# Kernel tuning notes

Hardware: AMD Instinct MI355X
Metric: run time of the kernel (lower is better)

Reference implementation:

```python
import jax, jax.numpy as jnp
import numpy as np
from jax import lax

C, CMID, RED, SCALE, KUP, KENC = 128, 64, 8, 2, 5, 3


def _conv(x, w, b=None, pad=0, groups=1):
    y = lax.conv_general_dilated(x, w, (1, 1), [(pad, pad), (pad, pad)],
                                 feature_group_count=groups,
                                 dimension_numbers=('NCHW', 'OIHW', 'NCHW'))
    if b is not None:
        y = y + b[None, :, None, None]
    return y


def setup_inputs() -> dict:
    key = jax.random.key(0)
    ks = jax.random.split(key, 8)
    s = 0.05
    return {
        'X': jax.random.normal(ks[0], (2, C, 64, 64), jnp.float32),
        'w3': jax.random.normal(ks[1], (CMID, C, 3, 3), jnp.float32) * s,
        'b3': jnp.zeros((CMID,), jnp.float32),
        'w5': jax.random.normal(ks[2], (CMID, C, 5, 5), jnp.float32) * s,
        'b5': jnp.zeros((CMID,), jnp.float32),
        'wa1': jax.random.normal(ks[3], (CMID // RED, CMID, 1, 1), jnp.float32) * s,
        'ba1': jnp.zeros((CMID // RED,), jnp.float32),
        'wa2': jax.random.normal(ks[4], (CMID, CMID // RED, 1, 1), jnp.float32) * s,
        'ba2': jnp.zeros((CMID,), jnp.float32),
        'wedge': jax.random.normal(ks[5], (CMID, 1, 3, 3), jnp.float32) * s,
        'wenc': jax.random.normal(ks[6], ((SCALE * KUP) ** 2, CMID, KENC, KENC), jnp.float32) * s,
    }


def reference(X, w3, b3, w5, b5, wa1, ba1, wa2, ba2, wedge, wenc):
    b, c, h, w = X.shape
    h_, w_ = h * SCALE, w * SCALE

    # kernel-prediction branch: 3x3 + 5x5 compression convs
    W = _conv(X, w3, b3, pad=1) + _conv(X, w5, b5, pad=2)

    # DetailEnhanceAttention: SE-style channel gate + depthwise edge conv
    avg = jnp.mean(W, axis=(2, 3), keepdims=True)            # (b, cmid, 1, 1)
    a = _conv(avg, wa1, ba1, pad=0)
    a = jax.nn.sigmoid(_conv(a, wa2, ba2, pad=0))
    edge = _conv(W, wedge, None, pad=1, groups=CMID)          # depthwise 3x3
    W = W * a + edge

    # encoder conv -> (b, (scale*k_up)^2, h, w)
    W = _conv(W, wenc, None, pad=KENC // 2)

    # PixelShuffle(scale): channels (k_up^2, r, r) -> (k_up^2, h*r, w*r)
    Wp = W.reshape(b, KUP * KUP, SCALE, SCALE, h, w)
    Wp = Wp.transpose(0, 1, 4, 2, 5, 3).reshape(b, KUP * KUP, h_, w_)
    Wp = jax.nn.softmax(Wp, axis=1)                           # softmax over k_up^2 taps

    # nearest upsample of X to (b, c, h_, w_)
    Xu = jnp.repeat(jnp.repeat(X, SCALE, axis=2), SCALE, axis=3)

    # unfold: kernel=k_up, dilation=scale, padding=k_up//2*scale
    p = (KUP // 2) * SCALE
    Xpad = jnp.pad(Xu, ((0, 0), (0, 0), (p, p), (p, p)))
    # (b, c, k_up^2, h_, w_), tap index = ki*k_up + kj (torch unfold order)
    patches = jnp.stack([
        Xpad[:, :, i * SCALE:i * SCALE + h_, j * SCALE:j * SCALE + w_]
        for i in range(KUP) for j in range(KUP)
    ], axis=2)

    out = jnp.einsum('bkhw,bckhw->bchw', Wp, patches)
    return out
```

## Files before the change

### kernel.cpp

```cpp
#include <hip/hip_runtime.h>
#include <math.h>

typedef __attribute__((ext_vector_type(2))) _Float16 f16x2;
typedef __attribute__((ext_vector_type(4))) _Float16 f16x4;
typedef __attribute__((ext_vector_type(8))) _Float16 f16x8;
typedef __attribute__((ext_vector_type(4))) float f32x4;

#if __has_builtin(__builtin_amdgcn_fdot2)
#define FDOT2(a, b, c) __builtin_amdgcn_fdot2((a), (b), (c), false)
#else
static __device__ __forceinline__ float FDOT2(f16x2 a, f16x2 b, float c) {
  return c + (float)a[0] * (float)b[0] + (float)a[1] * (float)b[1];
}
#endif

#define XPAD8_B  0
#define WFC_B    2506752
#define WFE_B    2916352
#define WFEATP_B 3045376
#define WEDGET_B 4194304
#define BCOMB_B  4195456
#define AVG_B    4195712

__global__ __launch_bounds__(256) void prep_kernel(
    const float* __restrict__ X,
    const float* __restrict__ w3, const float* __restrict__ b3,
    const float* __restrict__ w5, const float* __restrict__ b5,
    const float* __restrict__ wedge, const float* __restrict__ wenc,
    char* __restrict__ wsb) {
  int idx = blockIdx.x * 256 + threadIdx.x;
  if (idx < 156672) {
    int x = idx % 72;
    int t = idx / 72;
    int y = t % 68;
    int t2 = t / 68;
    int gg = t2 & 15, b = t2 >> 4;
    int yy = y - 2, xx = x - 2;
    bool ok = (yy >= 0 && yy < 64 && xx >= 0 && xx < 64);
    f16x8 h;
#pragma unroll
    for (int j = 0; j < 8; ++j) {
      float v = ok ? X[((b * 128 + gg * 8 + j) << 12) + yy * 64 + xx] : 0.f;
      h[j] = (_Float16)v;
    }
    ((f16x8*)(wsb + XPAD8_B))[idx] = h;
  }
  if (idx < 25600) {
    int l = idx & 63;
    int q = idx >> 6;
    int ntg = q & 3;
    int q2 = q >> 2;
    int cc = q2 & 3;
    int t = q2 >> 2;
    int ky = t / 5, kx = t % 5;
    int oc = ntg * 16 + (l & 15);
    int ci0 = cc * 32 + (l >> 4) * 8;
    f16x8 h;
#pragma unroll
    for (int i = 0; i < 8; ++i) {
      int ci = ci0 + i;
      float v = w5[(oc * 128 + ci) * 25 + t];
      if (ky >= 1 && ky <= 3 && kx >= 1 && kx <= 3)
        v += w3[(oc * 128 + ci) * 9 + (ky - 1) * 3 + (kx - 1)];
      h[i] = (_Float16)v;
    }
    ((f16x8*)(wsb + WFC_B))[idx] = h;
  }
  if (idx < 8064) {
    int l = idx & 63;
    int q = idx >> 6;
    int nt = q % 7;
    int q2 = q / 7;
    int cc = q2 & 1;
    int t = q2 >> 1;
    int oc = nt * 16 + (l & 15);
    int ci0 = cc * 32 + (l >> 4) * 8;
    f16x8 h;
#pragma unroll
    for (int i = 0; i < 8; ++i) {
      float v = (oc < 100) ? wenc[(oc * 64 + ci0 + i) * 9 + t] : 0.f;
      h[i] = (_Float16)v;
    }
    ((f16x8*)(wsb + WFE_B))[idx] = h;
  }
  if (idx < 6272) {
    int plane = idx / 392, p = idx % 392;
    int r, c;
    if (p < 136) {
      r = (p >= 68) ? 65 : 0;
      c = p % 68;
    } else {
      int q = p - 136;
      r = 1 + (q >> 2);
      int cm = q & 3;
      c = (cm == 0) ? 0 : (64 + cm);
    }
    f16x8 z = {(_Float16)0.f, (_Float16)0.f, (_Float16)0.f, (_Float16)0.f,
               (_Float16)0.f, (_Float16)0.f, (_Float16)0.f, (_Float16)0.f};
    *(f16x8*)((_Float16*)(wsb + WFEATP_B) + ((size_t)(plane * 66 + r) * 68 + c) * 8) = z;
  }
  if (idx < 72) {
    int k = idx >> 3, gg = idx & 7;
    f16x8 h;
#pragma unroll
    for (int j = 0; j < 8; ++j) h[j] = (_Float16)wedge[(gg * 8 + j) * 9 + k];
    ((f16x8*)(wsb + WEDGET_B))[idx] = h;
  }
  if (idx < 64) ((float*)(wsb + BCOMB_B))[idx] = b3[idx] + b5[idx];
  if (idx < 128) ((float*)(wsb + AVG_B))[idx] = b3[idx & 63] + b5[idx & 63];
}

__global__ __launch_bounds__(256) void convw_kernel(
    const _Float16* __restrict__ xpad8, const f16x8* __restrict__ wfc,
    const float* __restrict__ bcomb, _Float16* __restrict__ wfeatp,
    float* __restrict__ avg) {
  __shared__ __attribute__((aligned(16))) _Float16 xs[18560];
  __shared__ float red[64];
  const int tid = threadIdx.x;
  const int z = blockIdx.z;
  const int b = z >> 2, ntg = z & 3;
  const int tx0 = blockIdx.x * 8, ty0 = blockIdx.y * 8;

  for (int u = tid; u < 2304; u += 256) {
    int gg = u / 144;
    int rem = u - gg * 144;
    int r = rem / 12, c = rem - r * 12;
    f16x8 v = *(const f16x8*)&xpad8[((size_t)((b * 16 + gg) * 68 + ty0 + r) * 72 + tx0 + c) * 8];
    *(f16x8*)&xs[gg * 1160 + r * 96 + c * 8] = v;
  }
  __syncthreads();

  const int w = __builtin_amdgcn_readfirstlane(tid >> 6);
  const int l = tid & 63;
  const int lm = l & 15, lg = l >> 4;
  const int p = w * 16 + lm;
  const int abase = (p >> 3) * 96 + (p & 7) * 8;

  f32x4 accA = {0.f, 0.f, 0.f, 0.f}, accB = {0.f, 0.f, 0.f, 0.f};
  for (int dy = 0; dy < 5; ++dy) {
    for (int dx = 0; dx < 5; ++dx) {
      const int t = dy * 5 + dx;
      const int toff = abase + dy * 96 + dx * 8;
      const f16x8* wt = wfc + (t * 16 + ntg) * 64 + l;
#pragma unroll
      for (int cc = 0; cc < 4; ++cc) {
        f16x8 a = *(const f16x8*)&xs[(cc * 4 + lg) * 1160 + toff];
        f16x8 bb = wt[cc * 256];
        if (cc & 1)
          accB = __builtin_amdgcn_mfma_f32_16x16x32_f16(a, bb, accB, 0, 0, 0);
        else
          accA = __builtin_amdgcn_mfma_f32_16x16x32_f16(a, bb, accA, 0, 0, 0);
      }
    }
  }
  f32x4 acc = accA + accB;

  float s = acc[0] + acc[1] + acc[2] + acc[3];
  s += __shfl_xor(s, 16);
  s += __shfl_xor(s, 32);
  const float bias = bcomb[ntg * 16 + lm];
  __syncthreads();
#pragma unroll
  for (int r = 0; r < 4; ++r) {
    int pd = w * 16 + lg * 4 + r;
    xs[pd * 24 + lm] = (_Float16)(acc[r] + bias);
  }
  if (l < 16) red[w * 16 + lm] = s;
  __syncthreads();
  if (tid < 128) {
    int g2 = tid >> 6, pd = tid & 63;
    f16x8 v = *(const f16x8*)&xs[pd * 24 + g2 * 8];
    int gy = ty0 + (pd >> 3), gx = tx0 + (pd & 7);
    *(f16x8*)&wfeatp[((size_t)((b * 8 + ntg * 2 + g2) * 66 + 1 + gy) * 68 + 1 + gx) * 8] = v;
  }
  if (tid < 16) {
    float tot = red[tid] + red[16 + tid] + red[32 + tid] + red[48 + tid];
    atomicAdd(&avg[b * 64 + ntg * 16 + tid], tot * (1.f / 4096.f));
  }
}

#define SM_XT  0
#define SM_XSV 26880
#define SM_TS  34688
#define SM_SML 34688
#define SM_SMW 49536
#define SM_TOT 57216

__global__ __launch_bounds__(512) void enccarafe_kernel(
    const _Float16* __restrict__ wfeatp, const f16x8* __restrict__ wfe,
    const _Float16* __restrict__ xpad8, const f16x8* __restrict__ wedgeT,
    const float* __restrict__ wa1, const float* __restrict__ ba1,
    const float* __restrict__ wa2, const float* __restrict__ ba2,
    const float* __restrict__ avg, float* __restrict__ out) {
  __shared__ __attribute__((aligned(16))) char smem[SM_TOT];
  __shared__ f16x8 wedt[72];
  __shared__ float tlat[8];
  __shared__ float gsh[64];
  _Float16* xt = (_Float16*)(smem + SM_XT);
  _Float16* xsv = (_Float16*)(smem + SM_XSV);
  _Float16* ts = (_Float16*)(smem + SM_TS);
  float* sml = (float*)(smem + SM_SML);
  f16x2* smw2 = (f16x2*)(smem + SM_SMW);

  const int tid = threadIdx.x;
  const int b = blockIdx.z;
  const int tx0 = blockIdx.x * 8, ty0 = blockIdx.y * 4;

  for (int u = tid; u < 1664; u += 512) {
    int gg = u / 104;
    int rem = u - gg * 104;
    int r = rem / 13, c = rem - r * 13;
    f16x8 v = *(const f16x8*)&xpad8[((size_t)((b * 16 + gg) * 68 + ty0 + r) * 72 + tx0 + c) * 8];
    *(f16x8*)&xt[gg * 840 + r * 104 + c * 8] = v;
  }
  for (int u = tid; u < 768; u += 512) {
    int gg = u / 96;
    int rem = u - gg * 96;
    int r = rem / 12, c = rem - r * 12;
    int pr = ty0 - 1 + r, pc = tx0 - 1 + c;
    f16x8 v = {(_Float16)0.f, (_Float16)0.f, (_Float16)0.f, (_Float16)0.f,
               (_Float16)0.f, (_Float16)0.f, (_Float16)0.f, (_Float16)0.f};
    if (pr >= 0 && pr < 66 && pc >= 0 && pc < 68)
      v = *(const f16x8*)&wfeatp[((size_t)((b * 8 + gg) * 66 + pr) * 68 + pc) * 8];
    *(f16x8*)&ts[gg * 776 + r * 96 + c * 8] = v;
  }
  if (tid < 72) wedt[tid] = wedgeT[tid];
  if (tid < 8) {
    float s = ba1[tid];
    for (int i = 0; i < 64; ++i) s += wa1[tid * 64 + i] * avg[b * 64 + i];
    tlat[tid] = s;
  }
  __syncthreads();
  if (tid < 64) {
    float s = ba2[tid];
#pragma unroll
    for (int j = 0; j < 8; ++j) s += wa2[tid * 8 + j] * tlat[j];
    gsh[tid] = 1.f / (1.f + expf(-s));
  }
  __syncthreads();

  for (int u = tid; u < 480; u += 512) {
    int gg = u / 60;
    int rem = u - gg * 60;
    int r6 = rem / 10, c10 = rem - r6 * 10;
    int vy = ty0 - 1 + r6, vx = tx0 - 1 + c10;
    f16x8 res = {(_Float16)0.f, (_Float16)0.f, (_Float16)0.f, (_Float16)0.f,
                 (_Float16)0.f, (_Float16)0.f, (_Float16)0.f, (_Float16)0.f};
    if (vy >= 0 && vy < 64 && vx >= 0 && vx < 64) {
      float vout[8];
      f16x8 ctr = *(const f16x8*)&ts[gg * 776 + (r6 + 1) * 96 + (c10 + 1) * 8];
#pragma unroll
      for (int j = 0; j < 8; ++j) vout[j] = (float)ctr[j] * gsh[gg * 8 + j];
#pragma unroll
      for (int ky = 0; ky < 3; ++ky) {
#pragma unroll
        for (int kx = 0; kx < 3; ++kx) {
          int k = ky * 3 + kx;
          f16x8 tv = *(const f16x8*)&ts[gg * 776 + (r6 + ky) * 96 + (c10 + kx) * 8];
          f16x8 wv = wedt[k * 8 + gg];
#pragma unroll
          for (int j = 0; j < 8; ++j) vout[j] = fmaf((float)wv[j], (float)tv[j], vout[j]);
        }
      }
#pragma unroll
      for (int j = 0; j < 8; ++j) res[j] = (_Float16)vout[j];
    }
    *(f16x8*)&xsv[gg * 488 + r6 * 80 + c10 * 8] = res;
  }
  __syncthreads();

  {
    const int w = __builtin_amdgcn_readfirstlane(tid >> 6);
    const int l = tid & 63;
    const int pg = w & 1, hs = w >> 1;
    const int lm = l & 15, lg = l >> 4;
    const int p = pg * 16 + lm;
    const int abase = (p >> 3) * 80 + (p & 7) * 8;
    const int nt0 = hs * 2;
    const int ncnt = (hs == 3) ? 1 : 2;

    f32x4 a0 = {0.f, 0.f, 0.f, 0.f}, a1 = {0.f, 0.f, 0.f, 0.f};
    for (int dy = 0; dy < 3; ++dy) {
      for (int dx = 0; dx < 3; ++dx) {
        const int t = dy * 3 + dx;
        const int toff = abase + dy * 80 + dx * 8;
#pragma unroll
        for (int cc = 0; cc < 2; ++cc) {
          f16x8 a = *(const f16x8*)&xsv[(cc * 4 + lg) * 488 + toff];
          f16x8 b0 = wfe[((t * 2 + cc) * 7 + nt0) * 64 + l];
          a0 = __builtin_amdgcn_mfma_f32_16x16x32_f16(a, b0, a0, 0, 0, 0);
          if (ncnt == 2) {
            f16x8 b1 = wfe[((t * 2 + cc) * 7 + nt0 + 1) * 64 + l];
            a1 = __builtin_amdgcn_mfma_f32_16x16x32_f16(a, b1, a1, 0, 0, 0);
          }
        }
      }
    }
#pragma unroll
    for (int r = 0; r < 4; ++r) {
      int pd = pg * 16 + 4 * lg + r;
      sml[pd * 116 + nt0 * 16 + lm] = a0[r];
      if (ncnt == 2) sml[pd * 116 + (nt0 + 1) * 16 + lm] = a1[r];
    }
  }
  __syncthreads();

  if (tid < 128) {
    int pix = tid >> 2, sub = tid & 3;
    float lv[25];
    float m = -1e30f;
#pragma unroll
    for (int k = 0; k < 25; ++k) {
      lv[k] = sml[pix * 116 + k * 4 + sub];
      m = fmaxf(m, lv[k]);
    }
    float s = 0.f;
#pragma unroll
    for (int k = 0; k < 25; ++k) {
      lv[k] = __expf(lv[k] - m);
      s += lv[k];
    }
    float inv = 1.f / s;
#pragma unroll
    for (int ki = 0; ki < 5; ++ki) {
#pragma unroll
      for (int pr = 0; pr < 3; ++pr) {
        float wlo = lv[ki * 5 + 2 * pr] * inv;
        float whi = (2 * pr + 1 < 5) ? lv[ki * 5 + 2 * pr + 1] * inv : 0.f;
        f16x2 pk = {(_Float16)wlo, (_Float16)whi};
        smw2[((ki * 3 + pr) * 32 + pix) * 4 + sub] = pk;
      }
    }
  }
  __syncthreads();

  {
    const int slot = tid >> 5, pix = tid & 31;
    const int py = pix >> 3, px = pix & 7;
    const _Float16* xb = xt + slot * 840;

    float acc[4][8];
#pragma unroll
    for (int s = 0; s < 4; ++s)
#pragma unroll
      for (int j = 0; j < 8; ++j) acc[s][j] = 0.f;

    union U8 { f16x8 v; unsigned int u[4]; };
#pragma unroll
    for (int ki = 0; ki < 5; ++ki) {
      const _Float16* row = xb + (py + ki) * 104 + px * 8;
      U8 C[6];
#pragma unroll
      for (int c = 0; c < 6; ++c) C[c].v = *(const f16x8*)(row + c * 8);
#pragma unroll
      for (int pr = 0; pr < 3; ++pr) {
        const f16x2* wp = &smw2[((ki * 3 + pr) * 32 + pix) * 4];
        f16x2 w0 = wp[0], w1 = wp[1], w2 = wp[2], w3 = wp[3];
        const U8& A = C[2 * pr];
        const U8& B = C[2 * pr + 1];
#pragma unroll
        for (int k = 0; k < 4; ++k) {
          unsigned int lo = __builtin_amdgcn_perm(B.u[k], A.u[k], 0x05040100u);
          unsigned int hi = __builtin_amdgcn_perm(B.u[k], A.u[k], 0x07060302u);
          f16x2 xlo = __builtin_bit_cast(f16x2, lo);
          f16x2 xhi = __builtin_bit_cast(f16x2, hi);
          acc[0][2 * k] = FDOT2(w0, xlo, acc[0][2 * k]);
          acc[1][2 * k] = FDOT2(w1, xlo, acc[1][2 * k]);
          acc[2][2 * k] = FDOT2(w2, xlo, acc[2][2 * k]);
          acc[3][2 * k] = FDOT2(w3, xlo, acc[3][2 * k]);
          acc[0][2 * k + 1] = FDOT2(w0, xhi, acc[0][2 * k + 1]);
          acc[1][2 * k + 1] = FDOT2(w1, xhi, acc[1][2 * k + 1]);
          acc[2][2 * k + 1] = FDOT2(w2, xhi, acc[2][2 * k + 1]);
          acc[3][2 * k + 1] = FDOT2(w3, xhi, acc[3][2 * k + 1]);
        }
      }
    }
    int y0o = 2 * (ty0 + py), x0o = 2 * (tx0 + px);
#pragma unroll
    for (int j = 0; j < 8; ++j) {
      int c = slot * 8 + j;
      float* op = out + ((size_t)(b * 128 + c) * 128 + y0o) * 128 + x0o;
      float2 v0 = {acc[0][j], acc[1][j]};
      float2 v1 = {acc[2][j], acc[3][j]};
      *(float2*)op = v0;
      *(float2*)(op + 128) = v1;
    }
  }
}

extern "C" void kernel_launch(void* const* d_in, const int* in_sizes, int n_in,
                              void* d_out, int out_size, void* d_ws, size_t ws_size,
                              hipStream_t stream) {
  const float* X     = (const float*)d_in[0];
  const float* w3    = (const float*)d_in[1];
  const float* b3    = (const float*)d_in[2];
  const float* w5    = (const float*)d_in[3];
  const float* b5    = (const float*)d_in[4];
  const float* wa1   = (const float*)d_in[5];
  const float* ba1   = (const float*)d_in[6];
  const float* wa2   = (const float*)d_in[7];
  const float* ba2   = (const float*)d_in[8];
  const float* wedge = (const float*)d_in[9];
  const float* wenc  = (const float*)d_in[10];
  char* wsb = (char*)d_ws;
  float* out = (float*)d_out;

  _Float16* xpad8  = (_Float16*)(wsb + XPAD8_B);
  f16x8*    wfc    = (f16x8*)(wsb + WFC_B);
  f16x8*    wfe    = (f16x8*)(wsb + WFE_B);
  _Float16* wfeatp = (_Float16*)(wsb + WFEATP_B);
  f16x8*    wedgeT = (f16x8*)(wsb + WEDGET_B);
  float*    bcomb  = (float*)(wsb + BCOMB_B);
  float*    avg    = (float*)(wsb + AVG_B);

  prep_kernel<<<612, 256, 0, stream>>>(X, w3, b3, w5, b5, wedge, wenc, wsb);
  convw_kernel<<<dim3(8, 8, 8), 256, 0, stream>>>(xpad8, wfc, bcomb, wfeatp, avg);
  enccarafe_kernel<<<dim3(8, 16, 2), 512, 0, stream>>>(
      wfeatp, wfe, xpad8, wedgeT, wa1, ba1, wa2, ba2, avg, out);
}
```

Before: 47.65 us.

## Halve tile heights and split conv K across waves for more blocks

```diff
diff --git a/kernel.cpp b/kernel.cpp
--- a/kernel.cpp
+++ b/kernel.cpp
@@ -114,77 +114,86 @@
     const _Float16* __restrict__ xpad8, const f16x8* __restrict__ wfc,
     const float* __restrict__ bcomb, _Float16* __restrict__ wfeatp,
     float* __restrict__ avg) {
-  __shared__ __attribute__((aligned(16))) _Float16 xs[18560];
-  __shared__ float red[64];
+  __shared__ __attribute__((aligned(16))) _Float16 xs[16 * 776];
+  __shared__ float red[2][64][4];
+  __shared__ float redm[2][16];
   const int tid = threadIdx.x;
   const int z = blockIdx.z;
   const int b = z >> 2, ntg = z & 3;
-  const int tx0 = blockIdx.x * 8, ty0 = blockIdx.y * 8;
-
-  for (int u = tid; u < 2304; u += 256) {
-    int gg = u / 144;
-    int rem = u - gg * 144;
+  const int tx0 = blockIdx.x * 8, ty0 = blockIdx.y * 4;
+
+  for (int u = tid; u < 1536; u += 256) {
+    int gg = u / 96;
+    int rem = u - gg * 96;
     int r = rem / 12, c = rem - r * 12;
     f16x8 v = *(const f16x8*)&xpad8[((size_t)((b * 16 + gg) * 68 + ty0 + r) * 72 + tx0 + c) * 8];
-    *(f16x8*)&xs[gg * 1160 + r * 96 + c * 8] = v;
+    *(f16x8*)&xs[gg * 776 + r * 96 + c * 8] = v;
   }
   __syncthreads();
 
   const int w = __builtin_amdgcn_readfirstlane(tid >> 6);
   const int l = tid & 63;
+  const int pg = w & 1, kh = w >> 1;
   const int lm = l & 15, lg = l >> 4;
-  const int p = w * 16 + lm;
+  const int p = pg * 16 + lm;
   const int abase = (p >> 3) * 96 + (p & 7) * 8;
 
-  f32x4 accA = {0.f, 0.f, 0.f, 0.f}, accB = {0.f, 0.f, 0.f, 0.f};
+  f32x4 acc = {0.f, 0.f, 0.f, 0.f};
   for (int dy = 0; dy < 5; ++dy) {
     for (int dx = 0; dx < 5; ++dx) {
       const int t = dy * 5 + dx;
       const int toff = abase + dy * 96 + dx * 8;
-      const f16x8* wt = wfc + (t * 16 + ntg) * 64 + l;
-#pragma unroll
-      for (int cc = 0; cc < 4; ++cc) {
-        f16x8 a = *(const f16x8*)&xs[(cc * 4 + lg) * 1160 + toff];
-        f16x8 bb = wt[cc * 256];
-        if (cc & 1)
-          accB = __builtin_amdgcn_mfma_f32_16x16x32_f16(a, bb, accB, 0, 0, 0);
-        else
-          accA = __builtin_amdgcn_mfma_f32_16x16x32_f16(a, bb, accA, 0, 0, 0);
+#pragma unroll
+      for (int cc2 = 0; cc2 < 2; ++cc2) {
+        const int cc = kh * 2 + cc2;
+        f16x8 a = *(const f16x8*)&xs[(cc * 4 + lg) * 776 + toff];
+        f16x8 bb = wfc[((t * 4 + cc) * 4 + ntg) * 64 + l];
+        acc = __builtin_amdgcn_mfma_f32_16x16x32_f16(a, bb, acc, 0, 0, 0);
       }
     }
   }
-  f32x4 acc = accA + accB;
-
-  float s = acc[0] + acc[1] + acc[2] + acc[3];
-  s += __shfl_xor(s, 16);
-  s += __shfl_xor(s, 32);
-  const float bias = bcomb[ntg * 16 + lm];
-  __syncthreads();
-#pragma unroll
-  for (int r = 0; r < 4; ++r) {
-    int pd = w * 16 + lg * 4 + r;
-    xs[pd * 24 + lm] = (_Float16)(acc[r] + bias);
-  }
-  if (l < 16) red[w * 16 + lm] = s;
-  __syncthreads();
-  if (tid < 128) {
-    int g2 = tid >> 6, pd = tid & 63;
+
+  if (kh == 1) {
+#pragma unroll
+    for (int r = 0; r < 4; ++r) red[pg][l][r] = acc[r];
+  }
+  __syncthreads();
+  if (kh == 0) {
+#pragma unroll
+    for (int r = 0; r < 4; ++r) acc[r] += red[pg][l][r];
+    float s = acc[0] + acc[1] + acc[2] + acc[3];
+    s += __shfl_xor(s, 16);
+    s += __shfl_xor(s, 32);
+    if (lg == 0) redm[pg][lm] = s;
+    const float bias = bcomb[ntg * 16 + lm];
+#pragma unroll
+    for (int r = 0; r < 4; ++r) {
+      int pd = pg * 16 + lg * 4 + r;
+      xs[pd * 24 + lm] = (_Float16)(acc[r] + bias);
+    }
+  }
+  __syncthreads();
+  if (tid < 64) {
+    int pd = tid >> 1, g2 = tid & 1;
     f16x8 v = *(const f16x8*)&xs[pd * 24 + g2 * 8];
     int gy = ty0 + (pd >> 3), gx = tx0 + (pd & 7);
     *(f16x8*)&wfeatp[((size_t)((b * 8 + ntg * 2 + g2) * 66 + 1 + gy) * 68 + 1 + gx) * 8] = v;
   }
   if (tid < 16) {
-    float tot = red[tid] + red[16 + tid] + red[32 + tid] + red[48 + tid];
+    float tot = redm[0][tid] + redm[1][tid];
     atomicAdd(&avg[b * 64 + ntg * 16 + tid], tot * (1.f / 4096.f));
   }
 }
 
 #define SM_XT  0
-#define SM_XSV 26880
-#define SM_TS  34688
-#define SM_SML 34688
-#define SM_SMW 49536
-#define SM_TOT 57216
+#define SM_XSV 19968
+#define SM_TS  25216
+#define SM_SML 25216
+#define SM_SMW 32640
+#define SM_WED 36480
+#define SM_TLA 37632
+#define SM_GSH 37664
+#define SM_TOT 37920
 
 __global__ __launch_bounds__(512) void enccarafe_kernel(
     const _Float16* __restrict__ wfeatp, const f16x8* __restrict__ wfe,
@@ -193,36 +202,36 @@
     const float* __restrict__ wa2, const float* __restrict__ ba2,
     const float* __restrict__ avg, float* __restrict__ out) {
   __shared__ __attribute__((aligned(16))) char smem[SM_TOT];
-  __shared__ f16x8 wedt[72];
-  __shared__ float tlat[8];
-  __shared__ float gsh[64];
   _Float16* xt = (_Float16*)(smem + SM_XT);
   _Float16* xsv = (_Float16*)(smem + SM_XSV);
   _Float16* ts = (_Float16*)(smem + SM_TS);
   float* sml = (float*)(smem + SM_SML);
   f16x2* smw2 = (f16x2*)(smem + SM_SMW);
+  f16x8* wedt = (f16x8*)(smem + SM_WED);
+  float* tlat = (float*)(smem + SM_TLA);
+  float* gsh = (float*)(smem + SM_GSH);
 
   const int tid = threadIdx.x;
   const int b = blockIdx.z;
-  const int tx0 = blockIdx.x * 8, ty0 = blockIdx.y * 4;
-
-  for (int u = tid; u < 1664; u += 512) {
-    int gg = u / 104;
-    int rem = u - gg * 104;
+  const int tx0 = blockIdx.x * 8, ty0 = blockIdx.y * 2;
+
+  for (int u = tid; u < 1248; u += 512) {
+    int gg = u / 78;
+    int rem = u - gg * 78;
     int r = rem / 13, c = rem - r * 13;
     f16x8 v = *(const f16x8*)&xpad8[((size_t)((b * 16 + gg) * 68 + ty0 + r) * 72 + tx0 + c) * 8];
-    *(f16x8*)&xt[gg * 840 + r * 104 + c * 8] = v;
-  }
-  for (int u = tid; u < 768; u += 512) {
-    int gg = u / 96;
-    int rem = u - gg * 96;
+    *(f16x8*)&xt[gg * 624 + r * 104 + c * 8] = v;
+  }
+  for (int u = tid; u < 576; u += 512) {
+    int gg = u / 72;
+    int rem = u - gg * 72;
     int r = rem / 12, c = rem - r * 12;
     int pr = ty0 - 1 + r, pc = tx0 - 1 + c;
     f16x8 v = {(_Float16)0.f, (_Float16)0.f, (_Float16)0.f, (_Float16)0.f,
                (_Float16)0.f, (_Float16)0.f, (_Float16)0.f, (_Float16)0.f};
     if (pr >= 0 && pr < 66 && pc >= 0 && pc < 68)
       v = *(const f16x8*)&wfeatp[((size_t)((b * 8 + gg) * 66 + pr) * 68 + pc) * 8];
-    *(f16x8*)&ts[gg * 776 + r * 96 + c * 8] = v;
+    *(f16x8*)&ts[gg * 584 + r * 96 + c * 8] = v;
   }
   if (tid < 72) wedt[tid] = wedgeT[tid];
   if (tid < 8) {
@@ -239,16 +248,16 @@
   }
   __syncthreads();
 
-  for (int u = tid; u < 480; u += 512) {
-    int gg = u / 60;
-    int rem = u - gg * 60;
+  if (tid < 320) {
+    int gg = tid / 40;
+    int rem = tid - gg * 40;
     int r6 = rem / 10, c10 = rem - r6 * 10;
     int vy = ty0 - 1 + r6, vx = tx0 - 1 + c10;
     f16x8 res = {(_Float16)0.f, (_Float16)0.f, (_Float16)0.f, (_Float16)0.f,
                  (_Float16)0.f, (_Float16)0.f, (_Float16)0.f, (_Float16)0.f};
     if (vy >= 0 && vy < 64 && vx >= 0 && vx < 64) {
       float vout[8];
-      f16x8 ctr = *(const f16x8*)&ts[gg * 776 + (r6 + 1) * 96 + (c10 + 1) * 8];
+      f16x8 ctr = *(const f16x8*)&ts[gg * 584 + (r6 + 1) * 96 + (c10 + 1) * 8];
 #pragma unroll
       for (int j = 0; j < 8; ++j) vout[j] = (float)ctr[j] * gsh[gg * 8 + j];
 #pragma unroll
@@ -256,7 +265,7 @@
 #pragma unroll
         for (int kx = 0; kx < 3; ++kx) {
           int k = ky * 3 + kx;
-          f16x8 tv = *(const f16x8*)&ts[gg * 776 + (r6 + ky) * 96 + (c10 + kx) * 8];
+          f16x8 tv = *(const f16x8*)&ts[gg * 584 + (r6 + ky) * 96 + (c10 + kx) * 8];
           f16x8 wv = wedt[k * 8 + gg];
 #pragma unroll
           for (int j = 0; j < 8; ++j) vout[j] = fmaf((float)wv[j], (float)tv[j], vout[j]);
@@ -265,47 +274,39 @@
 #pragma unroll
       for (int j = 0; j < 8; ++j) res[j] = (_Float16)vout[j];
     }
-    *(f16x8*)&xsv[gg * 488 + r6 * 80 + c10 * 8] = res;
+    *(f16x8*)&xsv[gg * 328 + r6 * 80 + c10 * 8] = res;
   }
   __syncthreads();
 
   {
     const int w = __builtin_amdgcn_readfirstlane(tid >> 6);
     const int l = tid & 63;
-    const int pg = w & 1, hs = w >> 1;
-    const int lm = l & 15, lg = l >> 4;
-    const int p = pg * 16 + lm;
-    const int abase = (p >> 3) * 80 + (p & 7) * 8;
-    const int nt0 = hs * 2;
-    const int ncnt = (hs == 3) ? 1 : 2;
-
-    f32x4 a0 = {0.f, 0.f, 0.f, 0.f}, a1 = {0.f, 0.f, 0.f, 0.f};
-    for (int dy = 0; dy < 3; ++dy) {
-      for (int dx = 0; dx < 3; ++dx) {
-        const int t = dy * 3 + dx;
-        const int toff = abase + dy * 80 + dx * 8;
-#pragma unroll
-        for (int cc = 0; cc < 2; ++cc) {
-          f16x8 a = *(const f16x8*)&xsv[(cc * 4 + lg) * 488 + toff];
-          f16x8 b0 = wfe[((t * 2 + cc) * 7 + nt0) * 64 + l];
-          a0 = __builtin_amdgcn_mfma_f32_16x16x32_f16(a, b0, a0, 0, 0, 0);
-          if (ncnt == 2) {
-            f16x8 b1 = wfe[((t * 2 + cc) * 7 + nt0 + 1) * 64 + l];
-            a1 = __builtin_amdgcn_mfma_f32_16x16x32_f16(a, b1, a1, 0, 0, 0);
+    if (w < 7) {
+      const int nt = w;
+      const int lm = l & 15, lg = l >> 4;
+      const int abase = (lm >> 3) * 80 + (lm & 7) * 8;
+
+      f32x4 a0 = {0.f, 0.f, 0.f, 0.f};
+      for (int dy = 0; dy < 3; ++dy) {
+        for (int dx = 0; dx < 3; ++dx) {
+          const int t = dy * 3 + dx;
+          const int toff = abase + dy * 80 + dx * 8;
+#pragma unroll
+          for (int cc = 0; cc < 2; ++cc) {
+            f16x8 a = *(const f16x8*)&xsv[(cc * 4 + lg) * 328 + toff];
+            f16x8 b0 = wfe[((t * 2 + cc) * 7 + nt) * 64 + l];
+            a0 = __builtin_amdgcn_mfma_f32_16x16x32_f16(a, b0, a0, 0, 0, 0);
           }
         }
       }
-    }
-#pragma unroll
-    for (int r = 0; r < 4; ++r) {
-      int pd = pg * 16 + 4 * lg + r;
-      sml[pd * 116 + nt0 * 16 + lm] = a0[r];
-      if (ncnt == 2) sml[pd * 116 + (nt0 + 1) * 16 + lm] = a1[r];
-    }
-  }
-  __syncthreads();
-
-  if (tid < 128) {
+#pragma unroll
+      for (int r = 0; r < 4; ++r)
+        sml[(4 * lg + r) * 116 + nt * 16 + lm] = a0[r];
+    }
+  }
+  __syncthreads();
+
+  if (tid < 64) {
     int pix = tid >> 2, sub = tid & 3;
     float lv[25];
     float m = -1e30f;
@@ -328,20 +329,22 @@
         float wlo = lv[ki * 5 + 2 * pr] * inv;
         float whi = (2 * pr + 1 < 5) ? lv[ki * 5 + 2 * pr + 1] * inv : 0.f;
         f16x2 pk = {(_Float16)wlo, (_Float16)whi};
-        smw2[((ki * 3 + pr) * 32 + pix) * 4 + sub] = pk;
+        smw2[((ki * 3 + pr) * 16 + pix) * 4 + sub] = pk;
       }
     }
   }
   __syncthreads();
 
   {
-    const int slot = tid >> 5, pix = tid & 31;
+    const int slot = tid >> 5;
+    const int rem = tid & 31;
+    const int syh = rem >> 4, pix = rem & 15;
     const int py = pix >> 3, px = pix & 7;
-    const _Float16* xb = xt + slot * 840;
-
-    float acc[4][8];
-#pragma unroll
-    for (int s = 0; s < 4; ++s)
+    const _Float16* xb = xt + slot * 624;
+
+    float acc[2][8];
+#pragma unroll
+    for (int s = 0; s < 2; ++s)
 #pragma unroll
       for (int j = 0; j < 8; ++j) acc[s][j] = 0.f;
 
@@ -354,8 +357,8 @@
       for (int c = 0; c < 6; ++c) C[c].v = *(const f16x8*)(row + c * 8);
 #pragma unroll
       for (int pr = 0; pr < 3; ++pr) {
-        const f16x2* wp = &smw2[((ki * 3 + pr) * 32 + pix) * 4];
-        f16x2 w0 = wp[0], w1 = wp[1], w2 = wp[2], w3 = wp[3];
+        const f16x2* wp = &smw2[((ki * 3 + pr) * 16 + pix) * 4 + syh * 2];
+        f16x2 w0 = wp[0], w1 = wp[1];
         const U8& A = C[2 * pr];
         const U8& B = C[2 * pr + 1];
 #pragma unroll
@@ -366,24 +369,18 @@
           f16x2 xhi = __builtin_bit_cast(f16x2, hi);
           acc[0][2 * k] = FDOT2(w0, xlo, acc[0][2 * k]);
           acc[1][2 * k] = FDOT2(w1, xlo, acc[1][2 * k]);
-          acc[2][2 * k] = FDOT2(w2, xlo, acc[2][2 * k]);
-          acc[3][2 * k] = FDOT2(w3, xlo, acc[3][2 * k]);
           acc[0][2 * k + 1] = FDOT2(w0, xhi, acc[0][2 * k + 1]);
           acc[1][2 * k + 1] = FDOT2(w1, xhi, acc[1][2 * k + 1]);
-          acc[2][2 * k + 1] = FDOT2(w2, xhi, acc[2][2 * k + 1]);
-          acc[3][2 * k + 1] = FDOT2(w3, xhi, acc[3][2 * k + 1]);
         }
       }
     }
-    int y0o = 2 * (ty0 + py), x0o = 2 * (tx0 + px);
+    int y0o = 2 * (ty0 + py) + syh, x0o = 2 * (tx0 + px);
 #pragma unroll
     for (int j = 0; j < 8; ++j) {
       int c = slot * 8 + j;
       float* op = out + ((size_t)(b * 128 + c) * 128 + y0o) * 128 + x0o;
       float2 v0 = {acc[0][j], acc[1][j]};
-      float2 v1 = {acc[2][j], acc[3][j]};
       *(float2*)op = v0;
-      *(float2*)(op + 128) = v1;
     }
   }
 }
@@ -414,7 +411,7 @@
   float*    avg    = (float*)(wsb + AVG_B);
 
   prep_kernel<<<612, 256, 0, stream>>>(X, w3, b3, w5, b5, wedge, wenc, wsb);
-  convw_kernel<<<dim3(8, 8, 8), 256, 0, stream>>>(xpad8, wfc, bcomb, wfeatp, avg);
-  enccarafe_kernel<<<dim3(8, 16, 2), 512, 0, stream>>>(
+  convw_kernel<<<dim3(8, 16, 8), 256, 0, stream>>>(xpad8, wfc, bcomb, wfeatp, avg);
+  enccarafe_kernel<<<dim3(8, 32, 2), 512, 0, stream>>>(
       wfeatp, wfe, xpad8, wedgeT, wa1, ba1, wa2, ba2, avg, out);
 }
```

Result: faster. 42.16 us (-11.5%).
